# Kernel optimization log

Measured on AMD Instinct MI355X. Metric: run time of the kernel, lower is better.

## Reference

```python
import jax, jax.numpy as jnp
import numpy as np

B, NC, DC = 4, 1024, 256      # batch, codebook entries, codebook dim
K, L = 512, 128               # num_latents, latent_dim
NP, Q = 65536, 64             # query points, queries_dim
LH = 8                        # latent self-attn heads (dim_head 64)
LN_EPS = 1e-5


def _ln(x, g, b):
    m = jnp.mean(x, axis=-1, keepdims=True)
    v = jnp.var(x, axis=-1, keepdims=True)
    return (x - m) * jax.lax.rsqrt(v + LN_EPS) * g + b


def _attn(x, ctx, wq, wkv, wo, bo, h):
    # x: [b,n,dq], ctx: [b,j,dc]; wq: [dq, h*d], wkv: [dc, 2*h*d]
    b, n, _ = x.shape
    j = ctx.shape[1]
    d = wq.shape[1] // h
    q = (x @ wq).reshape(b, n, h, d)
    k, v = jnp.split(ctx @ wkv, 2, axis=-1)
    k = k.reshape(b, j, h, d)
    v = v.reshape(b, j, h, d)
    sim = jnp.einsum('bihd,bjhd->bhij', q, k) * (d ** -0.5)
    a = jax.nn.softmax(sim, axis=-1)
    o = jnp.einsum('bhij,bjhd->bihd', a, v).reshape(b, n, h * d)
    return o @ wo + bo


def _geglu(x):
    a, g = jnp.split(x, 2, axis=-1)
    return a * jax.nn.gelu(g, approximate=False)  # torch F.gelu is exact erf


def setup_inputs() -> dict:
    key = jax.random.key(0)
    ks = iter(jax.random.split(key, 32))
    def w(shape):  # kaiming-ish scaled randn, [in, out] layout
        return jax.random.normal(next(ks), shape, jnp.float32) / np.sqrt(shape[0]).astype(np.float32)
    inp = {
        'codebook': jax.random.normal(next(ks), (B, NC, DC), jnp.float32),
        'queries': jax.random.normal(next(ks), (B, NP, Q), jnp.float32),
        'latents': jax.random.normal(next(ks), (K, L), jnp.float32),
        # CodebookAttention: cross-attn (PreNorm with context norm)
        'ca_ng': jnp.ones((L,)), 'ca_nb': jnp.zeros((L,)),
        'ca_cng': jnp.ones((DC,)), 'ca_cnb': jnp.zeros((DC,)),
        'ca_wq': w((L, 64)), 'ca_wkv': w((DC, 128)), 'ca_wo': w((64, L)), 'ca_bo': jnp.zeros((L,)),
        # cross FF (GEGLU, mult=4)
        'cf_ng': jnp.ones((L,)), 'cf_nb': jnp.zeros((L,)),
        'cf_w1': w((L, 8 * L)), 'cf_b1': jnp.zeros((8 * L,)),
        'cf_w2': w((4 * L, L)), 'cf_b2': jnp.zeros((L,)),
        # latent self-attn (8 heads x 64)
        'sa_ng': jnp.ones((L,)), 'sa_nb': jnp.zeros((L,)),
        'sa_wq': w((L, 512)), 'sa_wkv': w((L, 1024)), 'sa_wo': w((512, L)), 'sa_bo': jnp.zeros((L,)),
        # self FF
        'sf_ng': jnp.ones((L,)), 'sf_nb': jnp.zeros((L,)),
        'sf_w1': w((L, 8 * L)), 'sf_b1': jnp.zeros((8 * L,)),
        'sf_w2': w((4 * L, L)), 'sf_b2': jnp.zeros((L,)),
        # CoordinateAttention: cross-attn
        'qa_ng': jnp.ones((Q,)), 'qa_nb': jnp.zeros((Q,)),
        'qa_cng': jnp.ones((L,)), 'qa_cnb': jnp.zeros((L,)),
        'qa_wq': w((Q, 64)), 'qa_wkv': w((L, 128)), 'qa_wo': w((64, Q)), 'qa_bo': jnp.zeros((Q,)),
        # decoder FF (geglu: hidden = 2*Q, GEGLU halves to Q)
        'qf_ng': jnp.ones((Q,)), 'qf_nb': jnp.zeros((Q,)),
        'qf_w1': w((Q, 2 * Q)), 'qf_b1': jnp.zeros((2 * Q,)),
        'qf_w2': w((Q, Q)), 'qf_b2': jnp.zeros((Q,)),
    }
    return inp


def reference(codebook, queries, latents,
              ca_ng, ca_nb, ca_cng, ca_cnb, ca_wq, ca_wkv, ca_wo, ca_bo,
              cf_ng, cf_nb, cf_w1, cf_b1, cf_w2, cf_b2,
              sa_ng, sa_nb, sa_wq, sa_wkv, sa_wo, sa_bo,
              sf_ng, sf_nb, sf_w1, sf_b1, sf_w2, sf_b2,
              qa_ng, qa_nb, qa_cng, qa_cnb, qa_wq, qa_wkv, qa_wo, qa_bo,
              qf_ng, qf_nb, qf_w1, qf_b1, qf_w2, qf_b2):
    b = codebook.shape[0]
    # ---- CodebookAttention ----
    x = jnp.broadcast_to(latents, (b,) + latents.shape)  # [b,K,L]
    xn = _ln(x, ca_ng, ca_nb)
    cn = _ln(codebook, ca_cng, ca_cnb)
    x = _attn(xn, cn, ca_wq, ca_wkv, ca_wo, ca_bo, 1) + x
    h = _ln(x, cf_ng, cf_nb)
    x = (_geglu(h @ cf_w1 + cf_b1) @ cf_w2 + cf_b2) + x
    xn = _ln(x, sa_ng, sa_nb)
    x = _attn(xn, xn, sa_wq, sa_wkv, sa_wo, sa_bo, LH) + x
    h = _ln(x, sf_ng, sf_nb)
    lat = (_geglu(h @ sf_w1 + sf_b1) @ sf_w2 + sf_b2) + x  # [b,K,L]
    # ---- CoordinateAttention ----
    y = queries  # [b,NP,Q]
    yn = _ln(y, qa_ng, qa_nb)
    cn = _ln(lat, qa_cng, qa_cnb)
    y = _attn(yn, cn, qa_wq, qa_wkv, qa_wo, qa_bo, 1) + y
    h = _ln(y, qf_ng, qf_nb)
    y = (_geglu(h @ qf_w1 + qf_b1) @ qf_w2 + qf_b2) + y
    return y
```

## Files before the change

### kernel.cpp

```cpp
#include <hip/hip_runtime.h>
#include <hip/hip_fp16.h>
#include <math.h>

#define DEV __device__ __forceinline__

typedef _Float16 f16x2 __attribute__((ext_vector_type(2)));

DEV float wsumf(float v){
  #pragma unroll
  for(int m=32;m>=1;m>>=1) v += __shfl_xor(v,m,64);
  return v;
}
DEV float wmaxf(float v){
  #pragma unroll
  for(int m=32;m>=1;m>>=1) v = fmaxf(v,__shfl_xor(v,m,64));
  return v;
}
DEV unsigned pk2(float a, float b){
  f16x2 h; h.x=(_Float16)a; h.y=(_Float16)b;
  return __builtin_bit_cast(unsigned, h);
}
DEV f16x2 u2h(unsigned u){ return __builtin_bit_cast(f16x2, u); }
DEV float fdot2f(f16x2 a, f16x2 b, float c){
#if __has_builtin(__builtin_amdgcn_fdot2)
  return __builtin_amdgcn_fdot2(a,b,c,false);
#else
  return c + (float)a.x*(float)b.x + (float)a.y*(float)b.y;
#endif
}
DEV float gelu_exact(float g){ return 0.5f*g*(1.f+erff(g*0.70710678118654752f)); }


__global__ void k_cb_kv(const float* __restrict__ cb, const float* __restrict__ cng,
                        const float* __restrict__ cnb, const float* __restrict__ wkv,
                        float* __restrict__ kcb, float* __restrict__ vcb){
  int r = blockIdx.x;
  int t = threadIdx.x;
  __shared__ float cn[256]; __shared__ float red[4];
  const float* row = cb + (size_t)r*256;
  float a0 = row[t], a1 = row[t+128];
  float s = wsumf(a0+a1), ss = wsumf(a0*a0+a1*a1);
  int w = t>>6;
  if ((t&63)==0){ red[w] = s; red[2+w] = ss; }
  __syncthreads();
  float mean = (red[0]+red[1])*(1.f/256.f);
  float var  = (red[2]+red[3])*(1.f/256.f) - mean*mean;
  float rstd = rsqrtf(var + 1e-5f);
  cn[t]     = (a0-mean)*rstd*cng[t]+cnb[t];
  cn[t+128] = (a1-mean)*rstd*cng[t+128]+cnb[t+128];
  __syncthreads();
  float acc = 0.f;
  for(int d=0; d<256; d++) acc += cn[d]*wkv[d*128+t];
  if (t<64) kcb[(size_t)r*64 + t] = acc;
  else      vcb[(size_t)r*64 + (t-64)] = acc;
}

__global__ void k_lat_q(const float* __restrict__ latents, const float* __restrict__ ng,
                        const float* __restrict__ nb, const float* __restrict__ wq,
                        float* __restrict__ q1){
  int i = blockIdx.x; int l = threadIdx.x;
  __shared__ float xn[128];
  float a0 = latents[i*128+l], a1 = latents[i*128+64+l];
  float s = wsumf(a0+a1), ss = wsumf(a0*a0+a1*a1);
  float mean = s*(1.f/128.f), var = ss*(1.f/128.f) - mean*mean;
  float rstd = rsqrtf(var+1e-5f);
  xn[l]    = (a0-mean)*rstd*ng[l]+nb[l];
  xn[64+l] = (a1-mean)*rstd*ng[64+l]+nb[64+l];
  __syncthreads();
  float acc=0.f;
  for(int d=0; d<128; d++) acc += xn[d]*wq[d*64+l];
  q1[i*64+l] = acc*0.125f;
}

__global__ void k_attn1(const float* __restrict__ q1, const float* __restrict__ kcb,
                        const float* __restrict__ vcb, const float* __restrict__ wo,
                        const float* __restrict__ bo, const float* __restrict__ latents,
                        float* __restrict__ x1){
  int b = blockIdx.y, i = blockIdx.x, l = threadIdx.x;
  __shared__ float qs[64], as[1024], os[64];
  qs[l] = q1[i*64+l];
  __syncthreads();
  float s[16];
  const float* kb = kcb + (size_t)b*1024*64;
  for(int t=0;t<16;t++){
    int j = l + 64*t; float acc=0.f;
    const float* kr = kb + (size_t)j*64;
    for(int d=0;d<64;d++) acc += qs[d]*kr[d];
    s[t]=acc;
  }
  float m=-1e30f;
  #pragma unroll
  for(int t=0;t<16;t++) m=fmaxf(m,s[t]);
  m=wmaxf(m);
  float sum=0.f;
  #pragma unroll
  for(int t=0;t<16;t++){ s[t]=__expf(s[t]-m); sum+=s[t]; }
  sum = wsumf(sum); float inv = 1.f/sum;
  #pragma unroll
  for(int t=0;t<16;t++) as[l+64*t] = s[t]*inv;
  __syncthreads();
  const float* vb = vcb + (size_t)b*1024*64;
  float o=0.f;
  for(int j=0;j<1024;j++) o += as[j]*vb[(size_t)j*64+l];
  os[l]=o; __syncthreads();
  float r0 = bo[l]    + latents[i*128+l];
  float r1 = bo[64+l] + latents[i*128+64+l];
  for(int d=0;d<64;d++){ float od=os[d]; r0 += od*wo[d*128+l]; r1 += od*wo[d*128+64+l]; }
  size_t ro = ((size_t)b*512+i)*128;
  x1[ro + l] = r0;
  x1[ro + 64+l] = r1;
}

__global__ void k_ffn(const float* __restrict__ xin, const float* __restrict__ ng,
                      const float* __restrict__ nb, const float* __restrict__ w1,
                      const float* __restrict__ b1, const float* __restrict__ w2,
                      const float* __restrict__ b2, float* __restrict__ xout){
  int r = blockIdx.x; int t = threadIdx.x;
  __shared__ float xi[128], h[128], tf[1024], red[8];
  const float* row = xin + (size_t)r*128;
  float a = (t<128)? row[t] : 0.f;
  float s=wsumf(a), ss=wsumf(a*a);
  int w=t>>6;
  if((t&63)==0){red[w]=s; red[4+w]=ss;}
  __syncthreads();
  float mean=(red[0]+red[1]+red[2]+red[3])*(1.f/128.f);
  float var =(red[4]+red[5]+red[6]+red[7])*(1.f/128.f) - mean*mean;
  float rstd=rsqrtf(var+1e-5f);
  if(t<128){ xi[t]=a; h[t]=(a-mean)*rstd*ng[t]+nb[t]; }
  __syncthreads();
  for(int c=t;c<1024;c+=256){
    float acc=b1[c];
    for(int d=0;d<128;d++) acc+=h[d]*w1[d*1024+c];
    tf[c]=acc;
  }
  __syncthreads();
  for(int c=t;c<512;c+=256){
    tf[c] = tf[c]*gelu_exact(tf[512+c]);
  }
  __syncthreads();
  if(t<128){
    float acc=b2[t];
    for(int d=0;d<512;d++) acc+=tf[d]*w2[d*128+t];
    xout[(size_t)r*128+t] = acc + xi[t];
  }
}

__global__ void k_sa_qkv(const float* __restrict__ xin, const float* __restrict__ ng,
                         const float* __restrict__ nb, const float* __restrict__ wq,
                         const float* __restrict__ wkv, float* __restrict__ saq,
                         float* __restrict__ sak, float* __restrict__ sav){
  int r=blockIdx.x, t=threadIdx.x;
  __shared__ float h[128], red[8];
  const float* row = xin + (size_t)r*128;
  float a = (t<128)? row[t]:0.f;
  float s=wsumf(a), ss=wsumf(a*a);
  int w=t>>6;
  if((t&63)==0){red[w]=s; red[4+w]=ss;}
  __syncthreads();
  float mean=(red[0]+red[1]+red[2]+red[3])*(1.f/128.f);
  float var =(red[4]+red[5]+red[6]+red[7])*(1.f/128.f)-mean*mean;
  float rstd=rsqrtf(var+1e-5f);
  if(t<128) h[t]=(a-mean)*rstd*ng[t]+nb[t];
  __syncthreads();
  for(int c=t;c<512;c+=256){
    float aq=0.f, ak=0.f, av=0.f;
    for(int d=0;d<128;d++){
      float hd=h[d];
      aq += hd*wq[d*512+c];
      ak += hd*wkv[d*1024+c];
      av += hd*wkv[d*1024+512+c];
    }
    size_t o=(size_t)r*512+c;
    saq[o]=aq*0.125f; sak[o]=ak; sav[o]=av;
  }
}

__global__ void k_sa_attn(const float* __restrict__ saq, const float* __restrict__ sak,
                          const float* __restrict__ sav, float* __restrict__ sao){
  int b=blockIdx.z, hh=blockIdx.y;
  int w=threadIdx.x>>6, l=threadIdx.x&63;
  int i=blockIdx.x*4+w;
  __shared__ float qs[4][64]; __shared__ float as[4][512];
  qs[w][l]=saq[((size_t)b*512+i)*512+hh*64+l];
  __syncthreads();
  const float* kb = sak + (size_t)b*512*512 + hh*64;
  float s[8];
  #pragma unroll
  for(int t=0;t<8;t++){
    int j=l+64*t; const float* kr=kb+(size_t)j*512; float acc=0.f;
    for(int d=0;d<64;d++) acc+=qs[w][d]*kr[d];
    s[t]=acc;
  }
  float m=-1e30f;
  #pragma unroll
  for(int t=0;t<8;t++) m=fmaxf(m,s[t]);
  m=wmaxf(m);
  float sum=0.f;
  #pragma unroll
  for(int t=0;t<8;t++){ s[t]=__expf(s[t]-m); sum+=s[t]; }
  sum=wsumf(sum);
  float inv=1.f/sum;
  #pragma unroll
  for(int t=0;t<8;t++) as[w][l+64*t]=s[t]*inv;
  __syncthreads();
  const float* vb = sav + (size_t)b*512*512 + hh*64;
  float o=0.f;
  for(int j=0;j<512;j++) o += as[w][j]*vb[(size_t)j*512+l];
  sao[((size_t)b*512+i)*512+hh*64+l]=o;
}

__global__ void k_sa_proj(const float* __restrict__ sao, const float* __restrict__ wo,
                          const float* __restrict__ bo, const float* __restrict__ resid,
                          float* __restrict__ xout){
  int r=blockIdx.x, t=threadIdx.x;
  __shared__ float o[512]; __shared__ float acc2[256];
  o[t]=sao[(size_t)r*512+t]; o[256+t]=sao[(size_t)r*512+256+t];
  __syncthreads();
  int c = t&127; int half = t>>7;
  float acc=0.f;
  int d0 = half*256;
  for(int d=d0; d<d0+256; d++) acc += o[d]*wo[d*128+c];
  acc2[t]=acc; __syncthreads();
  if(t<128) xout[(size_t)r*128+t] = acc2[t]+acc2[t+128]+bo[t]+resid[(size_t)r*128+t];
}

__global__ void k_kv2p(const float* __restrict__ lat, const float* __restrict__ cng,
                       const float* __restrict__ cnb, const float* __restrict__ wkv,
                       unsigned* __restrict__ kp, unsigned* __restrict__ vp){
  int r=blockIdx.x, t=threadIdx.x;
  __shared__ float cn[128]; __shared__ float red[4]; __shared__ float kv[128];
  float a = lat[(size_t)r*128+t];
  float s=wsumf(a), ss=wsumf(a*a);
  int w=t>>6;
  if((t&63)==0){red[w]=s;red[2+w]=ss;}
  __syncthreads();
  float mean=(red[0]+red[1])*(1.f/128.f), var=(red[2]+red[3])*(1.f/128.f)-mean*mean;
  float rstd=rsqrtf(var+1e-5f);
  cn[t]=(a-mean)*rstd*cng[t]+cnb[t];
  __syncthreads();
  float acc=0.f;
  for(int d=0;d<128;d++) acc+=cn[d]*wkv[d*128+t];
  kv[t]=acc;
  __syncthreads();
  if(t<32)               kp[(size_t)r*32 + t]      = pk2(kv[2*t],      kv[2*t+1]);
  else if(t>=64 && t<96) vp[(size_t)r*32 + (t-64)] = pk2(kv[64+2*(t-64)], kv[64+2*(t-64)+1]);
}

#define KLS 0
#define VLS 16384
#define GWQ 32768
#define WOP 34816
#define CSKo 36928
#define CNKo 37440
#define CSF 37952
#define CNF 38016
#define CS2 38080
#define CN2 38112
#define LDSU32 38144

__global__ void __launch_bounds__(512,1) k_coord_pt(
    const float* __restrict__ queries, const unsigned* __restrict__ kp_g,
    const unsigned* __restrict__ vp_g, const float* __restrict__ ng,
    const float* __restrict__ nb, const float* __restrict__ wq,
    const float* __restrict__ wo, const float* __restrict__ bo,
    float* __restrict__ out){
  extern __shared__ unsigned lds[];
  int tid=threadIdx.x;
  int b = blockIdx.x>>7;
  const unsigned* kg=kp_g+(size_t)b*16384;
  const unsigned* vg=vp_g+(size_t)b*16384;
  for(int idx=tid; idx<4096; idx+=512){
    ((uint4*)(lds+KLS))[idx]=((const uint4*)kg)[idx];
    ((uint4*)(lds+VLS))[idx]=((const uint4*)vg)[idx];
  }
  for(int idx=tid; idx<2048; idx+=512){
    int e2=idx>>6, d=idx&63;
    lds[GWQ+idx]=pk2(ng[2*e2]*wq[(2*e2)*64+d], ng[2*e2+1]*wq[(2*e2+1)*64+d]);
  }
  for(int idx=tid; idx<2112; idx+=512){
    int d2=idx>>6, r=idx&63;
    lds[WOP+idx]=(d2<32)? pk2(wo[(2*d2)*64+r], wo[(2*d2+1)*64+r]) : pk2(bo[r],0.f);
  }
  if(tid<64){
    float cs=0.f, cn=0.f;
    for(int e=0;e<64;e++){ float wv=wq[e*64+tid]; cs+=ng[e]*wv; cn+=nb[e]*wv; }
    ((float*)(lds+CSF))[tid]=cs; ((float*)(lds+CNF))[tid]=cn;
  }
  __syncthreads();
  if(tid<32){
    const float* csf=(const float*)(lds+CSF); const float* cnf=(const float*)(lds+CNF);
    lds[CS2+tid]=pk2(csf[2*tid],csf[2*tid+1]);
    lds[CN2+tid]=pk2(cnf[2*tid],cnf[2*tid+1]);
  }
  __syncthreads();
  {
    float a=0.f, c=0.f;
    #pragma unroll 1
    for(int d2=0; d2<32; d2++){
      f16x2 kk=u2h(lds[KLS + tid*32 + d2]);
      a=fdot2f(u2h(lds[CS2+d2]),kk,a);
      c=fdot2f(u2h(lds[CN2+d2]),kk,c);
    }
    ((float*)(lds+CSKo))[tid]=0.125f*a;
    ((float*)(lds+CNKo))[tid]=0.125f*c;
  }
  __syncthreads();

  size_t row=(size_t)blockIdx.x*512 + tid;
  const float* yr=queries+row*64;
  float ysum=0.f, ysq=0.f;
  unsigned yp2[32];
  {
    float4 yv[16];
    #pragma unroll
    for(int i=0;i<16;i++){
      yv[i]=((const float4*)yr)[i];
      ysum += (yv[i].x+yv[i].y)+(yv[i].z+yv[i].w);
      ysq  += yv[i].x*yv[i].x+yv[i].y*yv[i].y+yv[i].z*yv[i].z+yv[i].w*yv[i].w;
    }
    #pragma unroll
    for(int i=0;i<16;i++){
      yp2[2*i]  =pk2(yv[i].x,yv[i].y);
      yp2[2*i+1]=pk2(yv[i].z,yv[i].w);
    }
  }
  float mean=ysum*(1.f/64.f);
  float rstd=rsqrtf(ysq*(1.f/64.f)-mean*mean+1e-5f);
  float rm=rstd*mean;
  float rawq[64];
  #pragma unroll
  for(int d=0;d<64;d++) rawq[d]=0.f;
  #pragma unroll 1
  for(int e2=0;e2<32;e2++){
    const uint4* wr=(const uint4*)(lds+GWQ+e2*64);
    f16x2 ye=u2h(yp2[e2]);
    #pragma unroll
    for(int db=0;db<16;db++){
      uint4 w4=wr[db];
      rawq[4*db+0]=fdot2f(ye,u2h(w4.x),rawq[4*db+0]);
      rawq[4*db+1]=fdot2f(ye,u2h(w4.y),rawq[4*db+1]);
      rawq[4*db+2]=fdot2f(ye,u2h(w4.z),rawq[4*db+2]);
      rawq[4*db+3]=fdot2f(ye,u2h(w4.w),rawq[4*db+3]);
    }
  }
  unsigned rq2[32];
  float sc=0.125f*rstd;
  #pragma unroll
  for(int d2=0;d2<32;d2++) rq2[d2]=pk2(sc*rawq[2*d2],sc*rawq[2*d2+1]);
  const float* cskf=(const float*)(lds+CSKo);
  const float* cnkf=(const float*)(lds+CNKo);
  float m=-1e30f, lsum=0.f;
  f16x2 o2[33];
  #pragma unroll
  for(int d2=0;d2<32;d2++) o2[d2]=u2h(0u);
  #pragma unroll 1
  for(int c=0;c<32;c++){
    float s[16];
    #pragma unroll
    for(int jj=0;jj<16;jj++){
      int j=c*16+jj;
      const uint4* kr=(const uint4*)(lds+KLS+j*32);
      float a0=0.f,a1=0.f,a2=0.f,a3=0.f;
      #pragma unroll
      for(int db=0;db<8;db++){
        uint4 k4=kr[db];
        a0=fdot2f(u2h(rq2[4*db+0]),u2h(k4.x),a0);
        a1=fdot2f(u2h(rq2[4*db+1]),u2h(k4.y),a1);
        a2=fdot2f(u2h(rq2[4*db+2]),u2h(k4.z),a2);
        a3=fdot2f(u2h(rq2[4*db+3]),u2h(k4.w),a3);
      }
      s[jj]=((a0+a1)+(a2+a3)) - rm*cskf[j] + cnkf[j];
    }
    float cm=s[0];
    #pragma unroll
    for(int jj=1;jj<16;jj++) cm=fmaxf(cm,s[jj]);
    float mnew=fmaxf(m,cm);
    float f=__expf(m-mnew);
    m=mnew;
    f16x2 fh; fh.x=fh.y=(_Float16)f;
    #pragma unroll
    for(int d2=0;d2<32;d2++) o2[d2]*=fh;
    lsum*=f;
    #pragma unroll
    for(int jj=0;jj<16;jj++){
      float p=__expf(s[jj]-mnew);
      lsum+=p;
      f16x2 ph; ph.x=ph.y=(_Float16)p;
      const uint4* vr=(const uint4*)(lds+VLS+(c*16+jj)*32);
      #pragma unroll
      for(int db=0;db<8;db++){
        uint4 v4=vr[db];
        o2[4*db+0]+=u2h(v4.x)*ph;
        o2[4*db+1]+=u2h(v4.y)*ph;
        o2[4*db+2]+=u2h(v4.z)*ph;
        o2[4*db+3]+=u2h(v4.w)*ph;
      }
    }
  }
  {
    float invl=1.f/lsum;
    f16x2 ih; ih.x=ih.y=(_Float16)invl;
    #pragma unroll
    for(int d2=0;d2<32;d2++) o2[d2]*=ih;
    o2[32]=u2h(pk2(1.f,0.f));
  }
  float acc[64];
  #pragma unroll
  for(int r=0;r<64;r++) acc[r]=0.f;
  #pragma unroll 1
  for(int d2=0;d2<33;d2++){
    const uint4* wr=(const uint4*)(lds+WOP+d2*64);
    f16x2 od=o2[d2];
    #pragma unroll
    for(int db=0;db<16;db++){
      uint4 w4=wr[db];
      acc[4*db+0]=fdot2f(od,u2h(w4.x),acc[4*db+0]);
      acc[4*db+1]=fdot2f(od,u2h(w4.y),acc[4*db+1]);
      acc[4*db+2]=fdot2f(od,u2h(w4.z),acc[4*db+2]);
      acc[4*db+3]=fdot2f(od,u2h(w4.w),acc[4*db+3]);
    }
  }
  float* orow=out+row*64;
  #pragma unroll
  for(int i=0;i<16;i++){
    float4 yv=((const float4*)yr)[i];
    float4 st;
    st.x=acc[4*i+0]+yv.x; st.y=acc[4*i+1]+yv.y;
    st.z=acc[4*i+2]+yv.z; st.w=acc[4*i+3]+yv.w;
    ((float4*)orow)[i]=st;
  }
}

__global__ void __launch_bounds__(512,1) k_ffq2(
    float* __restrict__ y, const float* __restrict__ ng, const float* __restrict__ nb,
    const float* __restrict__ w1, const float* __restrict__ b1,
    const float* __restrict__ w2, const float* __restrict__ b2){
  __shared__ __align__(16) unsigned gw1p[4096];
  __shared__ __align__(16) unsigned w2p[2112];
  __shared__ float cs1f[128], cn1f[128];
  int tid=threadIdx.x;
  for(int idx=tid;idx<4096;idx+=512){
    int cc=idx>>5, e2=idx&31;
    gw1p[idx]=pk2(ng[2*e2]*w1[(2*e2)*128+cc], ng[2*e2+1]*w1[(2*e2+1)*128+cc]);
  }
  for(int idx=tid;idx<2112;idx+=512){
    int d2=idx>>6, r=idx&63;
    w2p[idx]=(d2<32)? pk2(w2[(2*d2)*64+r], w2[(2*d2+1)*64+r]) : pk2(b2[r],0.f);
  }
  if(tid<128){
    float cs=0.f, cn=0.f;
    for(int e=0;e<64;e++){ float wv=w1[e*128+tid]; cs+=ng[e]*wv; cn+=nb[e]*wv; }
    cs1f[tid]=cs; cn1f[tid]=cn+b1[tid];
  }
  __syncthreads();
  size_t row=(size_t)blockIdx.x*512 + tid;
  float* yrow=y+row*64;
  float ysum=0.f, ysq=0.f;
  unsigned yp2[32];
  {
    float4 yv[16];
    #pragma unroll
    for(int i=0;i<16;i++){
      yv[i]=((const float4*)yrow)[i];
      ysum += (yv[i].x+yv[i].y)+(yv[i].z+yv[i].w);
      ysq  += yv[i].x*yv[i].x+yv[i].y*yv[i].y+yv[i].z*yv[i].z+yv[i].w*yv[i].w;
    }
    float mean=ysum*(1.f/64.f);
    float rstd=rsqrtf(ysq*(1.f/64.f)-mean*mean+1e-5f);
    float rm=rstd*mean;
    #pragma unroll
    for(int i=0;i<16;i++){
      yp2[2*i]  =pk2(rstd*yv[i].x,rstd*yv[i].y);
      yp2[2*i+1]=pk2(rstd*yv[i].z,rstd*yv[i].w);
    }
    ysum=rm;
  }
  float rm=ysum;
  unsigned u2[33];
  #pragma unroll 1
  for(int c=0;c<64;c+=2){
    float uu[2];
    #pragma unroll
    for(int k=0;k<2;k++){
      int cc=c+k;
      const uint4* wa=(const uint4*)&gw1p[cc*32];
      const uint4* wg=(const uint4*)&gw1p[(cc+64)*32];
      float a0=0.f,a1=0.f,g0=0.f,g1=0.f;
      #pragma unroll
      for(int db=0;db<8;db++){
        uint4 A=wa[db], G=wg[db];
        a0=fdot2f(u2h(yp2[4*db+0]),u2h(A.x),a0);
        a1=fdot2f(u2h(yp2[4*db+1]),u2h(A.y),a1);
        a0=fdot2f(u2h(yp2[4*db+2]),u2h(A.z),a0);
        a1=fdot2f(u2h(yp2[4*db+3]),u2h(A.w),a1);
        g0=fdot2f(u2h(yp2[4*db+0]),u2h(G.x),g0);
        g1=fdot2f(u2h(yp2[4*db+1]),u2h(G.y),g1);
        g0=fdot2f(u2h(yp2[4*db+2]),u2h(G.z),g0);
        g1=fdot2f(u2h(yp2[4*db+3]),u2h(G.w),g1);
      }
      float ha=(a0+a1)-rm*cs1f[cc]+cn1f[cc];
      float hg=(g0+g1)-rm*cs1f[cc+64]+cn1f[cc+64];
      uu[k]=ha*gelu_exact(hg);
    }
    u2[c>>1]=pk2(uu[0],uu[1]);
  }
  u2[32]=pk2(1.f,0.f);
  float acc[64];
  #pragma unroll
  for(int r=0;r<64;r++) acc[r]=0.f;
  #pragma unroll 1
  for(int d2=0;d2<33;d2++){
    const uint4* wr=(const uint4*)&w2p[d2*64];
    f16x2 ud=u2h(u2[d2]);
    #pragma unroll
    for(int db=0;db<16;db++){
      uint4 w4=wr[db];
      acc[4*db+0]=fdot2f(ud,u2h(w4.x),acc[4*db+0]);
      acc[4*db+1]=fdot2f(ud,u2h(w4.y),acc[4*db+1]);
      acc[4*db+2]=fdot2f(ud,u2h(w4.z),acc[4*db+2]);
      acc[4*db+3]=fdot2f(ud,u2h(w4.w),acc[4*db+3]);
    }
  }
  #pragma unroll
  for(int i=0;i<16;i++){
    float4 yv=((const float4*)yrow)[i];
    float4 st;
    st.x=acc[4*i+0]+yv.x; st.y=acc[4*i+1]+yv.y;
    st.z=acc[4*i+2]+yv.z; st.w=acc[4*i+3]+yv.w;
    ((float4*)yrow)[i]=st;
  }
}

extern "C" void kernel_launch(void* const* d_in, const int* in_sizes, int n_in,
                              void* d_out, int out_size, void* d_ws, size_t ws_size,
                              hipStream_t stream){
  const float* cb      =(const float*)d_in[0];
  const float* queries =(const float*)d_in[1];
  const float* latents =(const float*)d_in[2];
  const float* ca_ng=(const float*)d_in[3],  *ca_nb=(const float*)d_in[4];
  const float* ca_cng=(const float*)d_in[5], *ca_cnb=(const float*)d_in[6];
  const float* ca_wq=(const float*)d_in[7],  *ca_wkv=(const float*)d_in[8];
  const float* ca_wo=(const float*)d_in[9],  *ca_bo=(const float*)d_in[10];
  const float* cf_ng=(const float*)d_in[11], *cf_nb=(const float*)d_in[12];
  const float* cf_w1=(const float*)d_in[13], *cf_b1=(const float*)d_in[14];
  const float* cf_w2=(const float*)d_in[15], *cf_b2=(const float*)d_in[16];
  const float* sa_ng=(const float*)d_in[17], *sa_nb=(const float*)d_in[18];
  const float* sa_wq=(const float*)d_in[19], *sa_wkv=(const float*)d_in[20];
  const float* sa_wo=(const float*)d_in[21], *sa_bo=(const float*)d_in[22];
  const float* sf_ng=(const float*)d_in[23], *sf_nb=(const float*)d_in[24];
  const float* sf_w1=(const float*)d_in[25], *sf_b1=(const float*)d_in[26];
  const float* sf_w2=(const float*)d_in[27], *sf_b2=(const float*)d_in[28];
  const float* qa_ng=(const float*)d_in[29], *qa_nb=(const float*)d_in[30];
  const float* qa_cng=(const float*)d_in[31],*qa_cnb=(const float*)d_in[32];
  const float* qa_wq=(const float*)d_in[33], *qa_wkv=(const float*)d_in[34];
  const float* qa_wo=(const float*)d_in[35], *qa_bo=(const float*)d_in[36];
  const float* qf_ng=(const float*)d_in[37], *qf_nb=(const float*)d_in[38];
  const float* qf_w1=(const float*)d_in[39], *qf_b1=(const float*)d_in[40];
  const float* qf_w2=(const float*)d_in[41], *qf_b2=(const float*)d_in[42];
  float* out=(float*)d_out;

  float* kcb = out;
  float* vcb = kcb + 262144;
  float* q1  = vcb + 262144;
  float* x1  = q1  + 32768;
  float* x2  = x1  + 262144;
  float* x3  = x2  + 262144;
  float* lat = x3  + 262144;
  float* saq = lat + 262144;
  float* sak = saq + 1048576;
  float* sav = sak + 1048576;
  float* sao = sav + 1048576;

  unsigned* kp=(unsigned*)d_ws;
  unsigned* vp=kp+65536;

  k_cb_kv<<<4096,128,0,stream>>>(cb,ca_cng,ca_cnb,ca_wkv,kcb,vcb);
  k_lat_q<<<512,64,0,stream>>>(latents,ca_ng,ca_nb,ca_wq,q1);
  k_attn1<<<dim3(512,4),64,0,stream>>>(q1,kcb,vcb,ca_wo,ca_bo,latents,x1);
  k_ffn<<<2048,256,0,stream>>>(x1,cf_ng,cf_nb,cf_w1,cf_b1,cf_w2,cf_b2,x2);
  k_sa_qkv<<<2048,256,0,stream>>>(x2,sa_ng,sa_nb,sa_wq,sa_wkv,saq,sak,sav);
  k_sa_attn<<<dim3(128,8,4),256,0,stream>>>(saq,sak,sav,sao);
  k_sa_proj<<<2048,256,0,stream>>>(sao,sa_wo,sa_bo,x2,x3);
  k_ffn<<<2048,256,0,stream>>>(x3,sf_ng,sf_nb,sf_w1,sf_b1,sf_w2,sf_b2,lat);
  k_kv2p<<<2048,128,0,stream>>>(lat,qa_cng,qa_cnb,qa_wkv,kp,vp);
  hipFuncSetAttribute((const void*)k_coord_pt,
                      hipFuncAttributeMaxDynamicSharedMemorySize, LDSU32*4);
  k_coord_pt<<<512,512,LDSU32*4,stream>>>(queries,kp,vp,qa_ng,qa_nb,qa_wq,qa_wo,qa_bo,out);
  k_ffq2<<<512,512,0,stream>>>(out,qf_ng,qf_nb,qf_w1,qf_b1,qf_w2,qf_b2);
}
```

Baseline: 1.811 ms.

## Read packed K/V and weights from global instead of LDS, prepack weights once

The coordinate attention and query FFN kernels stop staging the per-batch K/V tables and packed weights into LDS. They instead read them directly from global memory through cache, with a one-block pre-pass kernel that packs the fp16 weight pairs. The LayerNorm gain is folded into the query activations rather than the weights, and biases seed the accumulators instead of using an extra packed row. The first cross-attention kernel is widened to 256 threads with a block-level softmax reduction. The aim is to free LDS and raise occupancy, at the cost of relying on L1/L2 to serve the K/V reads that every thread repeats.

```diff
diff --git a/kernel.cpp b/kernel.cpp
--- a/kernel.cpp
+++ b/kernel.cpp
@@ -76,39 +76,48 @@
                         const float* __restrict__ vcb, const float* __restrict__ wo,
                         const float* __restrict__ bo, const float* __restrict__ latents,
                         float* __restrict__ x1){
-  int b = blockIdx.y, i = blockIdx.x, l = threadIdx.x;
-  __shared__ float qs[64], as[1024], os[64];
-  qs[l] = q1[i*64+l];
-  __syncthreads();
-  float s[16];
-  const float* kb = kcb + (size_t)b*1024*64;
-  for(int t=0;t<16;t++){
-    int j = l + 64*t; float acc=0.f;
+  int b = blockIdx.y, i = blockIdx.x, t = threadIdx.x;
+  int l = t&63, w = t>>6;
+  __shared__ float qs[64], as[1024], red[4][64], redm[4], reds[4], os[64];
+  if(t<64) qs[t] = q1[i*64+t];
+  __syncthreads();
+  const float* kb = kcb + (size_t)b*65536;
+  float s[4];
+  #pragma unroll
+  for(int tt=0;tt<4;tt++){
+    int j = t + 256*tt; float acc=0.f;
     const float* kr = kb + (size_t)j*64;
     for(int d=0;d<64;d++) acc += qs[d]*kr[d];
-    s[t]=acc;
-  }
-  float m=-1e30f;
-  #pragma unroll
-  for(int t=0;t<16;t++) m=fmaxf(m,s[t]);
-  m=wmaxf(m);
+    s[tt]=acc;
+  }
+  float m = fmaxf(fmaxf(s[0],s[1]),fmaxf(s[2],s[3]));
+  m = wmaxf(m);
+  if(l==0) redm[w]=m;
+  __syncthreads();
+  m = fmaxf(fmaxf(redm[0],redm[1]),fmaxf(redm[2],redm[3]));
   float sum=0.f;
   #pragma unroll
-  for(int t=0;t<16;t++){ s[t]=__expf(s[t]-m); sum+=s[t]; }
-  sum = wsumf(sum); float inv = 1.f/sum;
-  #pragma unroll
-  for(int t=0;t<16;t++) as[l+64*t] = s[t]*inv;
-  __syncthreads();
-  const float* vb = vcb + (size_t)b*1024*64;
+  for(int tt=0;tt<4;tt++){ s[tt]=__expf(s[tt]-m); sum+=s[tt]; }
+  sum = wsumf(sum);
+  if(l==0) reds[w]=sum;
+  __syncthreads();
+  sum = reds[0]+reds[1]+reds[2]+reds[3];
+  float inv = 1.f/sum;
+  #pragma unroll
+  for(int tt=0;tt<4;tt++) as[t+256*tt] = s[tt]*inv;
+  __syncthreads();
+  const float* vb = vcb + (size_t)b*65536;
   float o=0.f;
-  for(int j=0;j<1024;j++) o += as[j]*vb[(size_t)j*64+l];
-  os[l]=o; __syncthreads();
-  float r0 = bo[l]    + latents[i*128+l];
-  float r1 = bo[64+l] + latents[i*128+64+l];
-  for(int d=0;d<64;d++){ float od=os[d]; r0 += od*wo[d*128+l]; r1 += od*wo[d*128+64+l]; }
-  size_t ro = ((size_t)b*512+i)*128;
-  x1[ro + l] = r0;
-  x1[ro + 64+l] = r1;
+  for(int j=256*w;j<256*w+256;j++) o += as[j]*vb[(size_t)j*64+l];
+  red[w][l]=o;
+  __syncthreads();
+  if(t<64) os[t]=red[0][t]+red[1][t]+red[2][t]+red[3][t];
+  __syncthreads();
+  if(t<128){
+    float r = bo[t] + latents[i*128+t];
+    for(int d=0;d<64;d++) r += os[d]*wo[d*128+t];
+    x1[((size_t)b*512+i)*128+t] = r;
+  }
 }
 
 __global__ void k_ffn(const float* __restrict__ xin, const float* __restrict__ ng,
@@ -246,70 +255,66 @@
   else if(t>=64 && t<96) vp[(size_t)r*32 + (t-64)] = pk2(kv[64+2*(t-64)], kv[64+2*(t-64)+1]);
 }
 
-#define KLS 0
-#define VLS 16384
-#define GWQ 32768
-#define WOP 34816
-#define CSKo 36928
-#define CNKo 37440
-#define CSF 37952
-#define CNF 38016
-#define CS2 38080
-#define CN2 38112
-#define LDSU32 38144
-
-__global__ void __launch_bounds__(512,1) k_coord_pt(
+__global__ void k_wpack(const float* __restrict__ wq, const float* __restrict__ wo,
+                        const float* __restrict__ w1, const float* __restrict__ w2,
+                        unsigned* __restrict__ wqp, unsigned* __restrict__ wop,
+                        unsigned* __restrict__ w1p, unsigned* __restrict__ w2p){
+  int tid=threadIdx.x;
+  for(int idx=tid; idx<2048; idx+=512){
+    int e2=idx>>6, d=idx&63;
+    wqp[idx]=pk2(wq[(2*e2)*64+d], wq[(2*e2+1)*64+d]);
+    wop[idx]=pk2(wo[(2*e2)*64+d], wo[(2*e2+1)*64+d]);
+    w2p[idx]=pk2(w2[(2*e2)*64+d], w2[(2*e2+1)*64+d]);
+  }
+  for(int idx=tid; idx<4096; idx+=512){
+    int c=idx>>5, e2=idx&31;
+    w1p[idx]=pk2(w1[(2*e2)*128+c], w1[(2*e2+1)*128+c]);
+  }
+}
+
+__global__ void __launch_bounds__(512) k_coord_pt(
     const float* __restrict__ queries, const unsigned* __restrict__ kp_g,
     const unsigned* __restrict__ vp_g, const float* __restrict__ ng,
     const float* __restrict__ nb, const float* __restrict__ wq,
-    const float* __restrict__ wo, const float* __restrict__ bo,
-    float* __restrict__ out){
-  extern __shared__ unsigned lds[];
+    const unsigned* __restrict__ wqp, const unsigned* __restrict__ wop,
+    const float* __restrict__ bo, float* __restrict__ out){
+  __shared__ float cskL[512], cnkL[512];
+  __shared__ float csf[64], cnf[64];
+  __shared__ unsigned cs2[32], cn2[32];
+  __shared__ float gL[64], boL[64];
   int tid=threadIdx.x;
   int b = blockIdx.x>>7;
   const unsigned* kg=kp_g+(size_t)b*16384;
   const unsigned* vg=vp_g+(size_t)b*16384;
-  for(int idx=tid; idx<4096; idx+=512){
-    ((uint4*)(lds+KLS))[idx]=((const uint4*)kg)[idx];
-    ((uint4*)(lds+VLS))[idx]=((const uint4*)vg)[idx];
-  }
-  for(int idx=tid; idx<2048; idx+=512){
-    int e2=idx>>6, d=idx&63;
-    lds[GWQ+idx]=pk2(ng[2*e2]*wq[(2*e2)*64+d], ng[2*e2+1]*wq[(2*e2+1)*64+d]);
-  }
-  for(int idx=tid; idx<2112; idx+=512){
-    int d2=idx>>6, r=idx&63;
-    lds[WOP+idx]=(d2<32)? pk2(wo[(2*d2)*64+r], wo[(2*d2+1)*64+r]) : pk2(bo[r],0.f);
-  }
   if(tid<64){
+    gL[tid]=ng[tid]; boL[tid]=bo[tid];
     float cs=0.f, cn=0.f;
     for(int e=0;e<64;e++){ float wv=wq[e*64+tid]; cs+=ng[e]*wv; cn+=nb[e]*wv; }
-    ((float*)(lds+CSF))[tid]=cs; ((float*)(lds+CNF))[tid]=cn;
+    csf[tid]=cs; cnf[tid]=cn;
   }
   __syncthreads();
   if(tid<32){
-    const float* csf=(const float*)(lds+CSF); const float* cnf=(const float*)(lds+CNF);
-    lds[CS2+tid]=pk2(csf[2*tid],csf[2*tid+1]);
-    lds[CN2+tid]=pk2(cnf[2*tid],cnf[2*tid+1]);
+    cs2[tid]=pk2(csf[2*tid],csf[2*tid+1]);
+    cn2[tid]=pk2(cnf[2*tid],cnf[2*tid+1]);
   }
   __syncthreads();
   {
     float a=0.f, c=0.f;
     #pragma unroll 1
     for(int d2=0; d2<32; d2++){
-      f16x2 kk=u2h(lds[KLS + tid*32 + d2]);
-      a=fdot2f(u2h(lds[CS2+d2]),kk,a);
-      c=fdot2f(u2h(lds[CN2+d2]),kk,c);
-    }
-    ((float*)(lds+CSKo))[tid]=0.125f*a;
-    ((float*)(lds+CNKo))[tid]=0.125f*c;
+      f16x2 kk=u2h(kg[tid*32+d2]);
+      a=fdot2f(u2h(cs2[d2]),kk,a);
+      c=fdot2f(u2h(cn2[d2]),kk,c);
+    }
+    cskL[tid]=0.125f*a;
+    cnkL[tid]=0.125f*c;
   }
   __syncthreads();
 
   size_t row=(size_t)blockIdx.x*512 + tid;
   const float* yr=queries+row*64;
   float ysum=0.f, ysq=0.f;
-  unsigned yp2[32];
+  unsigned ypg[32];
   {
     float4 yv[16];
     #pragma unroll
@@ -318,22 +323,23 @@
       ysum += (yv[i].x+yv[i].y)+(yv[i].z+yv[i].w);
       ysq  += yv[i].x*yv[i].x+yv[i].y*yv[i].y+yv[i].z*yv[i].z+yv[i].w*yv[i].w;
     }
+    float mean=ysum*(1.f/64.f);
+    float rstd=rsqrtf(ysq*(1.f/64.f)-mean*mean+1e-5f);
+    ysum=rstd*mean;
     #pragma unroll
     for(int i=0;i<16;i++){
-      yp2[2*i]  =pk2(yv[i].x,yv[i].y);
-      yp2[2*i+1]=pk2(yv[i].z,yv[i].w);
-    }
-  }
-  float mean=ysum*(1.f/64.f);
-  float rstd=rsqrtf(ysq*(1.f/64.f)-mean*mean+1e-5f);
-  float rm=rstd*mean;
+      ypg[2*i]  =pk2(rstd*yv[i].x*gL[4*i],   rstd*yv[i].y*gL[4*i+1]);
+      ypg[2*i+1]=pk2(rstd*yv[i].z*gL[4*i+2], rstd*yv[i].w*gL[4*i+3]);
+    }
+  }
+  float rm=ysum;
   float rawq[64];
   #pragma unroll
   for(int d=0;d<64;d++) rawq[d]=0.f;
   #pragma unroll 1
   for(int e2=0;e2<32;e2++){
-    const uint4* wr=(const uint4*)(lds+GWQ+e2*64);
-    f16x2 ye=u2h(yp2[e2]);
+    const uint4* wr=(const uint4*)(wqp+e2*64);
+    f16x2 ye=u2h(ypg[e2]);
     #pragma unroll
     for(int db=0;db<16;db++){
       uint4 w4=wr[db];
@@ -344,22 +350,19 @@
     }
   }
   unsigned rq2[32];
-  float sc=0.125f*rstd;
-  #pragma unroll
-  for(int d2=0;d2<32;d2++) rq2[d2]=pk2(sc*rawq[2*d2],sc*rawq[2*d2+1]);
-  const float* cskf=(const float*)(lds+CSKo);
-  const float* cnkf=(const float*)(lds+CNKo);
+  #pragma unroll
+  for(int d2=0;d2<32;d2++) rq2[d2]=pk2(0.125f*rawq[2*d2],0.125f*rawq[2*d2+1]);
   float m=-1e30f, lsum=0.f;
-  f16x2 o2[33];
+  f16x2 o2[32];
   #pragma unroll
   for(int d2=0;d2<32;d2++) o2[d2]=u2h(0u);
   #pragma unroll 1
-  for(int c=0;c<32;c++){
-    float s[16];
-    #pragma unroll
-    for(int jj=0;jj<16;jj++){
-      int j=c*16+jj;
-      const uint4* kr=(const uint4*)(lds+KLS+j*32);
+  for(int c=0;c<64;c++){
+    float s[8];
+    #pragma unroll
+    for(int jj=0;jj<8;jj++){
+      int j=c*8+jj;
+      const uint4* kr=(const uint4*)(kg+(size_t)j*32);
       float a0=0.f,a1=0.f,a2=0.f,a3=0.f;
       #pragma unroll
       for(int db=0;db<8;db++){
@@ -369,24 +372,23 @@
         a2=fdot2f(u2h(rq2[4*db+2]),u2h(k4.z),a2);
         a3=fdot2f(u2h(rq2[4*db+3]),u2h(k4.w),a3);
       }
-      s[jj]=((a0+a1)+(a2+a3)) - rm*cskf[j] + cnkf[j];
+      s[jj]=((a0+a1)+(a2+a3)) - rm*cskL[j] + cnkL[j];
     }
     float cm=s[0];
     #pragma unroll
-    for(int jj=1;jj<16;jj++) cm=fmaxf(cm,s[jj]);
-    float mnew=fmaxf(m,cm);
-    float f=__expf(m-mnew);
-    m=mnew;
+    for(int jj=1;jj<8;jj++) cm=fmaxf(cm,s[jj]);
+    float mn=fmaxf(m,cm);
+    float f=__expf(m-mn); m=mn;
     f16x2 fh; fh.x=fh.y=(_Float16)f;
     #pragma unroll
     for(int d2=0;d2<32;d2++) o2[d2]*=fh;
     lsum*=f;
     #pragma unroll
-    for(int jj=0;jj<16;jj++){
-      float p=__expf(s[jj]-mnew);
-      lsum+=p;
-      f16x2 ph; ph.x=ph.y=(_Float16)p;
-      const uint4* vr=(const uint4*)(lds+VLS+(c*16+jj)*32);
+    for(int jj=0;jj<8;jj++){ s[jj]=__expf(s[jj]-mn); lsum+=s[jj]; }
+    #pragma unroll
+    for(int jj=0;jj<8;jj++){
+      const uint4* vr=(const uint4*)(vg+(size_t)(c*8+jj)*32);
+      f16x2 ph; ph.x=ph.y=(_Float16)s[jj];
       #pragma unroll
       for(int db=0;db<8;db++){
         uint4 v4=vr[db];
@@ -402,14 +404,13 @@
     f16x2 ih; ih.x=ih.y=(_Float16)invl;
     #pragma unroll
     for(int d2=0;d2<32;d2++) o2[d2]*=ih;
-    o2[32]=u2h(pk2(1.f,0.f));
   }
   float acc[64];
   #pragma unroll
-  for(int r=0;r<64;r++) acc[r]=0.f;
-  #pragma unroll 1
-  for(int d2=0;d2<33;d2++){
-    const uint4* wr=(const uint4*)(lds+WOP+d2*64);
+  for(int r=0;r<64;r++) acc[r]=boL[r];
+  #pragma unroll
+  for(int d2=0;d2<32;d2++){
+    const uint4* wr=(const uint4*)(wop+d2*64);
     f16x2 od=o2[d2];
     #pragma unroll
     for(int db=0;db<16;db++){
@@ -431,22 +432,15 @@
   }
 }
 
-__global__ void __launch_bounds__(512,1) k_ffq2(
+__global__ void __launch_bounds__(512) k_ffq2(
     float* __restrict__ y, const float* __restrict__ ng, const float* __restrict__ nb,
     const float* __restrict__ w1, const float* __restrict__ b1,
-    const float* __restrict__ w2, const float* __restrict__ b2){
-  __shared__ __align__(16) unsigned gw1p[4096];
-  __shared__ __align__(16) unsigned w2p[2112];
+    const unsigned* __restrict__ w1p, const unsigned* __restrict__ w2p,
+    const float* __restrict__ b2){
   __shared__ float cs1f[128], cn1f[128];
+  __shared__ float gL[64], b2L[64];
   int tid=threadIdx.x;
-  for(int idx=tid;idx<4096;idx+=512){
-    int cc=idx>>5, e2=idx&31;
-    gw1p[idx]=pk2(ng[2*e2]*w1[(2*e2)*128+cc], ng[2*e2+1]*w1[(2*e2+1)*128+cc]);
-  }
-  for(int idx=tid;idx<2112;idx+=512){
-    int d2=idx>>6, r=idx&63;
-    w2p[idx]=(d2<32)? pk2(w2[(2*d2)*64+r], w2[(2*d2+1)*64+r]) : pk2(b2[r],0.f);
-  }
+  if(tid<64){ gL[tid]=ng[tid]; b2L[tid]=b2[tid]; }
   if(tid<128){
     float cs=0.f, cn=0.f;
     for(int e=0;e<64;e++){ float wv=w1[e*128+tid]; cs+=ng[e]*wv; cn+=nb[e]*wv; }
@@ -456,7 +450,7 @@
   size_t row=(size_t)blockIdx.x*512 + tid;
   float* yrow=y+row*64;
   float ysum=0.f, ysq=0.f;
-  unsigned yp2[32];
+  unsigned ypg[32];
   {
     float4 yv[16];
     #pragma unroll
@@ -467,36 +461,35 @@
     }
     float mean=ysum*(1.f/64.f);
     float rstd=rsqrtf(ysq*(1.f/64.f)-mean*mean+1e-5f);
-    float rm=rstd*mean;
+    ysum=rstd*mean;
     #pragma unroll
     for(int i=0;i<16;i++){
-      yp2[2*i]  =pk2(rstd*yv[i].x,rstd*yv[i].y);
-      yp2[2*i+1]=pk2(rstd*yv[i].z,rstd*yv[i].w);
-    }
-    ysum=rm;
+      ypg[2*i]  =pk2(rstd*yv[i].x*gL[4*i],   rstd*yv[i].y*gL[4*i+1]);
+      ypg[2*i+1]=pk2(rstd*yv[i].z*gL[4*i+2], rstd*yv[i].w*gL[4*i+3]);
+    }
   }
   float rm=ysum;
-  unsigned u2[33];
-  #pragma unroll 1
+  unsigned u2[32];
+  #pragma unroll
   for(int c=0;c<64;c+=2){
     float uu[2];
     #pragma unroll
     for(int k=0;k<2;k++){
       int cc=c+k;
-      const uint4* wa=(const uint4*)&gw1p[cc*32];
-      const uint4* wg=(const uint4*)&gw1p[(cc+64)*32];
+      const uint4* wa=(const uint4*)(w1p+cc*32);
+      const uint4* wg=(const uint4*)(w1p+(cc+64)*32);
       float a0=0.f,a1=0.f,g0=0.f,g1=0.f;
       #pragma unroll
       for(int db=0;db<8;db++){
         uint4 A=wa[db], G=wg[db];
-        a0=fdot2f(u2h(yp2[4*db+0]),u2h(A.x),a0);
-        a1=fdot2f(u2h(yp2[4*db+1]),u2h(A.y),a1);
-        a0=fdot2f(u2h(yp2[4*db+2]),u2h(A.z),a0);
-        a1=fdot2f(u2h(yp2[4*db+3]),u2h(A.w),a1);
-        g0=fdot2f(u2h(yp2[4*db+0]),u2h(G.x),g0);
-        g1=fdot2f(u2h(yp2[4*db+1]),u2h(G.y),g1);
-        g0=fdot2f(u2h(yp2[4*db+2]),u2h(G.z),g0);
-        g1=fdot2f(u2h(yp2[4*db+3]),u2h(G.w),g1);
+        a0=fdot2f(u2h(ypg[4*db+0]),u2h(A.x),a0);
+        a1=fdot2f(u2h(ypg[4*db+1]),u2h(A.y),a1);
+        a0=fdot2f(u2h(ypg[4*db+2]),u2h(A.z),a0);
+        a1=fdot2f(u2h(ypg[4*db+3]),u2h(A.w),a1);
+        g0=fdot2f(u2h(ypg[4*db+0]),u2h(G.x),g0);
+        g1=fdot2f(u2h(ypg[4*db+1]),u2h(G.y),g1);
+        g0=fdot2f(u2h(ypg[4*db+2]),u2h(G.z),g0);
+        g1=fdot2f(u2h(ypg[4*db+3]),u2h(G.w),g1);
       }
       float ha=(a0+a1)-rm*cs1f[cc]+cn1f[cc];
       float hg=(g0+g1)-rm*cs1f[cc+64]+cn1f[cc+64];
@@ -504,13 +497,12 @@
     }
     u2[c>>1]=pk2(uu[0],uu[1]);
   }
-  u2[32]=pk2(1.f,0.f);
   float acc[64];
   #pragma unroll
-  for(int r=0;r<64;r++) acc[r]=0.f;
-  #pragma unroll 1
-  for(int d2=0;d2<33;d2++){
-    const uint4* wr=(const uint4*)&w2p[d2*64];
+  for(int r=0;r<64;r++) acc[r]=b2L[r];
+  #pragma unroll
+  for(int d2=0;d2<32;d2++){
+    const uint4* wr=(const uint4*)(w2p+d2*64);
     f16x2 ud=u2h(u2[d2]);
     #pragma unroll
     for(int db=0;db<16;db++){
@@ -571,20 +563,23 @@
   float* sav = sak + 1048576;
   float* sao = sav + 1048576;
 
-  unsigned* kp=(unsigned*)d_ws;
-  unsigned* vp=kp+65536;
-
+  unsigned* kp =(unsigned*)d_ws;
+  unsigned* vp = kp+65536;
+  unsigned* wqp= vp+65536;
+  unsigned* wop= wqp+2048;
+  unsigned* w1p= wop+2048;
+  unsigned* w2p= w1p+4096;
+
+  k_wpack<<<1,512,0,stream>>>(qa_wq,qa_wo,qf_w1,qf_w2,wqp,wop,w1p,w2p);
   k_cb_kv<<<4096,128,0,stream>>>(cb,ca_cng,ca_cnb,ca_wkv,kcb,vcb);
   k_lat_q<<<512,64,0,stream>>>(latents,ca_ng,ca_nb,ca_wq,q1);
-  k_attn1<<<dim3(512,4),64,0,stream>>>(q1,kcb,vcb,ca_wo,ca_bo,latents,x1);
+  k_attn1<<<dim3(512,4),256,0,stream>>>(q1,kcb,vcb,ca_wo,ca_bo,latents,x1);
   k_ffn<<<2048,256,0,stream>>>(x1,cf_ng,cf_nb,cf_w1,cf_b1,cf_w2,cf_b2,x2);
   k_sa_qkv<<<2048,256,0,stream>>>(x2,sa_ng,sa_nb,sa_wq,sa_wkv,saq,sak,sav);
   k_sa_attn<<<dim3(128,8,4),256,0,stream>>>(saq,sak,sav,sao);
   k_sa_proj<<<2048,256,0,stream>>>(sao,sa_wo,sa_bo,x2,x3);
   k_ffn<<<2048,256,0,stream>>>(x3,sf_ng,sf_nb,sf_w1,sf_b1,sf_w2,sf_b2,lat);
   k_kv2p<<<2048,128,0,stream>>>(lat,qa_cng,qa_cnb,qa_wkv,kp,vp);
-  hipFuncSetAttribute((const void*)k_coord_pt,
-                      hipFuncAttributeMaxDynamicSharedMemorySize, LDSU32*4);
-  k_coord_pt<<<512,512,LDSU32*4,stream>>>(queries,kp,vp,qa_ng,qa_nb,qa_wq,qa_wo,qa_bo,out);
-  k_ffq2<<<512,512,0,stream>>>(out,qf_ng,qf_nb,qf_w1,qf_b1,qf_w2,qf_b2);
-}
+  k_coord_pt<<<512,512,0,stream>>>(queries,kp,vp,qa_ng,qa_nb,qa_wq,wqp,wop,qa_bo,out);
+  k_ffq2<<<512,512,0,stream>>>(out,qf_ng,qf_nb,qf_w1,qf_b1,w1p,w2p,qf_b2);
+}
```

Measured after the change: 1.904 ms. 5.1% more time.
